# Kernel optimization log

Measured on AMD Instinct MI355X. Metric: run time of the kernel, lower is better.

The kernel has to match this reference:

```python
import jax, jax.numpy as jnp
import numpy as np

SEQ_LEN = 8192
HEAD_DIM = 128


def setup_inputs() -> dict:
    key = jax.random.key(0)
    kq, kk, kv = jax.random.split(key, 3)
    q = jax.random.normal(kq, (SEQ_LEN, HEAD_DIM), dtype=jnp.float32)
    k = jax.random.normal(kk, (SEQ_LEN, HEAD_DIM), dtype=jnp.float32)
    v = jax.random.normal(kv, (SEQ_LEN, HEAD_DIM), dtype=jnp.float32)
    return {"q": q, "k": k, "v": v}


def reference(q, k, v):
    # FlashAttention computes exact softmax attention; the blocked loops with
    # online max/sum rescaling in the source are an exact reformulation of:
    #   O = softmax(Q K^T) V
    # NOTE: the original module applies no 1/sqrt(d) scaling, so neither do we.
    s = jnp.einsum('nd,md->nm', q, k)          # [N, N] scores
    p = jax.nn.softmax(s, axis=-1)             # stable softmax (online in src)
    return jnp.einsum('nm,md->nd', p, v)       # [N, d]
```

## Files before the change

kernel.cpp:

```cpp
#include <hip/hip_runtime.h>

#define N_SEQ 8192
#define HDIM  128

typedef _Float16 half8v  __attribute__((ext_vector_type(8)));
typedef float    floatx16 __attribute__((ext_vector_type(16)));
typedef unsigned int uint32;

__global__ void prep_kv(const float* __restrict__ K, const float* __restrict__ V,
                        _Float16* __restrict__ K16s, _Float16* __restrict__ Vs) {
    __shared__ float Kl[32 * 132];
    __shared__ float Vl[32 * 132];
    const int t  = threadIdx.x;
    const int nt = blockIdx.x;
    const int n0 = nt * 32;
    #pragma unroll
    for (int kk = 0; kk < 4; kk++) {
        int idx = t + 256 * kk;
        int nl = idx >> 5, c4 = idx & 31;
        float4 f = *(((const float4*)(K + (size_t)(n0 + nl) * HDIM)) + c4);
        float* dk = &Kl[nl * 132 + c4 * 4];
        dk[0] = f.x; dk[1] = f.y; dk[2] = f.z; dk[3] = f.w;
        float4 g = *(((const float4*)(V + (size_t)(n0 + nl) * HDIM)) + c4);
        float* dv = &Vl[nl * 132 + c4 * 4];
        dv[0] = g.x; dv[1] = g.y; dv[2] = g.z; dv[3] = g.w;
    }
    __syncthreads();
    #pragma unroll
    for (int rep = 0; rep < 2; rep++) {
        int ch = t + rep * 256;
        int kc = ch >> 6, lane = ch & 63, l31 = lane & 31, q5 = (lane >> 5) & 1;
        half8v h;
        #pragma unroll
        for (int j = 0; j < 8; j++) h[j] = (_Float16)Kl[l31 * 132 + kc * 16 + q5 * 8 + j];
        *(half8v*)(K16s + (((size_t)nt * 8 + kc) * 64 + lane) * 8) = h;
    }
    #pragma unroll
    for (int rep = 0; rep < 2; rep++) {
        int ch = t + rep * 256;
        int dt = ch >> 7, kc2 = (ch >> 6) & 1, lane = ch & 63, l31 = lane & 31, q5 = (lane >> 5) & 1;
        half8v h;
        #pragma unroll
        for (int j = 0; j < 8; j++) h[j] = (_Float16)Vl[(kc2 * 16 + q5 * 8 + j) * 132 + dt * 32 + l31];
        *(half8v*)(Vs + ((((size_t)nt * 4 + dt) * 2 + kc2) * 64 + lane) * 8) = h;
    }
}

static __device__ __forceinline__ void stage_tile(
        const _Float16* __restrict__ K16s, const _Float16* __restrict__ Vs,
        _Float16* lds, size_t nt, int wv, int lane) {
    #pragma unroll
    for (int i = 0; i < 4; i++) {
        const int c = wv * 4 + i;
        const _Float16* base = (c < 8) ? (K16s + (nt * 8 + c) * 512)
                                       : (Vs + (nt * 8 + (size_t)(c - 8)) * 512);
        __builtin_amdgcn_global_load_lds(
            (const __attribute__((address_space(1))) void*)(base + lane * 8),
            (__attribute__((address_space(3))) void*)(lds + c * 512),
            16, 0, 0);
    }
}

static __device__ __forceinline__ void do_pv(const half8v (&vsrc)[8], const uint32 (&hpk)[8],
                                             floatx16 (&oacc)[4], int q5) {
    #pragma unroll
    for (int kc2 = 0; kc2 < 2; kc2++) {
        uint32 pass0 = q5 ? hpk[4 * kc2 + 0] : hpk[4 * kc2 + 2];
        uint32 pass1 = q5 ? hpk[4 * kc2 + 1] : hpk[4 * kc2 + 3];
        uint32 r0 = (uint32)__shfl_xor((int)pass0, 32, 64);
        uint32 r1 = (uint32)__shfl_xor((int)pass1, 32, 64);
        uint32 b0 = q5 ? r0 : hpk[4 * kc2 + 0];
        uint32 b1 = q5 ? r1 : hpk[4 * kc2 + 1];
        uint32 b2 = q5 ? hpk[4 * kc2 + 2] : r0;
        uint32 b3 = q5 ? hpk[4 * kc2 + 3] : r1;
        uint4 bu = make_uint4(b0, b1, b2, b3);
        half8v bfrag = __builtin_bit_cast(half8v, bu);
        #pragma unroll
        for (int dt = 0; dt < 4; dt++)
            oacc[dt] = __builtin_amdgcn_mfma_f32_32x32x16_f16(vsrc[dt * 2 + kc2], bfrag, oacc[dt], 0, 0, 0);
    }
}

template <bool DO_PV>
static __device__ __forceinline__ void pipe_step(
        const half8v (&qf)[8], half8v (&vin)[8], const half8v (&vprev)[8],
        floatx16 (&oacc)[4], uint32 (&hpk)[8],
        float& runm, float& lsum, float& palpha, bool& pflag,
        const _Float16* lds, int lane, int q5) {
    half8v kf[8];
    #pragma unroll
    for (int kc = 0; kc < 8; kc++)
        kf[kc] = *(const half8v*)(lds + kc * 512 + lane * 8);
    #pragma unroll
    for (int j = 0; j < 8; j++)
        vin[j] = *(const half8v*)(lds + (8 + j) * 512 + lane * 8);
    if (pflag) {
        #pragma unroll
        for (int dt = 0; dt < 4; dt++)
            #pragma unroll
            for (int r = 0; r < 16; r++) oacc[dt][r] *= palpha;
        pflag = false;
    }
    if (DO_PV) do_pv(vprev, hpk, oacc, q5);
    floatx16 s0, s1;
    #pragma unroll
    for (int r = 0; r < 16; r++) { s0[r] = 0.0f; s1[r] = 0.0f; }
    #pragma unroll
    for (int kc = 0; kc < 4; kc++)
        s0 = __builtin_amdgcn_mfma_f32_32x32x16_f16(kf[kc], qf[kc], s0, 0, 0, 0);
    #pragma unroll
    for (int kc = 4; kc < 8; kc++)
        s1 = __builtin_amdgcn_mfma_f32_32x32x16_f16(kf[kc], qf[kc], s1, 0, 0, 0);
    float sc[16];
    #pragma unroll
    for (int r = 0; r < 16; r++) sc[r] = s0[r] + s1[r];
    float tm[8];
    #pragma unroll
    for (int r = 0; r < 8; r++) tm[r] = fmaxf(sc[r], sc[r + 8]);
    #pragma unroll
    for (int w = 4; w; w >>= 1)
        #pragma unroll
        for (int r = 0; r < w; r++) tm[r] = fmaxf(tm[r], tm[r + w]);
    float cmax = fmaxf(tm[0], __shfl_xor(tm[0], 32, 64));
    if (__any(cmax > runm + 12.0f)) {
        const float mnew = fmaxf(runm, cmax);
        palpha = __builtin_amdgcn_exp2f(runm - mnew);
        runm = mnew;
        lsum *= palpha;
        pflag = true;
    }
    float p[16];
    #pragma unroll
    for (int r = 0; r < 16; r++) p[r] = __builtin_amdgcn_exp2f(sc[r] - runm);
    float ts[8];
    #pragma unroll
    for (int r = 0; r < 8; r++) ts[r] = p[r] + p[r + 8];
    #pragma unroll
    for (int w = 4; w; w >>= 1)
        #pragma unroll
        for (int r = 0; r < w; r++) ts[r] += ts[r + w];
    lsum += ts[0];
    #pragma unroll
    for (int t2 = 0; t2 < 8; t2++) {
        auto pk = __builtin_amdgcn_cvt_pkrtz(p[2 * t2], p[2 * t2 + 1]);
        hpk[t2] = __builtin_bit_cast(uint32, pk);
    }
}

__launch_bounds__(256, 2)
__global__ void fa_main(const float* __restrict__ Qp, const _Float16* __restrict__ K16s,
                        const _Float16* __restrict__ Vs, float* __restrict__ Opart,
                        float* __restrict__ lpart, float* __restrict__ mpart, int tiles) {
    __shared__ _Float16 ldsbuf[2][8192];
    const int tid  = threadIdx.x;
    const int lane = tid & 63;
    const int wv   = tid >> 6;
    const int l31  = lane & 31;
    const int q5   = lane >> 5;
    const int sp   = blockIdx.x;
    const int m0   = blockIdx.y * 128 + wv * 32;
    const float LOG2E = 1.44269504088896f;

    half8v qf[8];
    {
        const float* qrow = Qp + (size_t)(m0 + l31) * HDIM;
        #pragma unroll
        for (int kc = 0; kc < 8; kc++) {
            const float4 a = *(const float4*)(qrow + kc * 16 + q5 * 8);
            const float4 b = *(const float4*)(qrow + kc * 16 + q5 * 8 + 4);
            half8v h;
            h[0] = (_Float16)(a.x * LOG2E); h[1] = (_Float16)(a.y * LOG2E);
            h[2] = (_Float16)(a.z * LOG2E); h[3] = (_Float16)(a.w * LOG2E);
            h[4] = (_Float16)(b.x * LOG2E); h[5] = (_Float16)(b.y * LOG2E);
            h[6] = (_Float16)(b.z * LOG2E); h[7] = (_Float16)(b.w * LOG2E);
            qf[kc] = h;
        }
    }

    floatx16 oacc[4];
    #pragma unroll
    for (int dt = 0; dt < 4; dt++)
        #pragma unroll
        for (int r = 0; r < 16; r++) oacc[dt][r] = 0.0f;

    float runm = -3.0e38f;
    float lsum = 0.0f;
    float palpha = 0.0f;
    bool  pflag = false;
    uint32 hpk[8];
    half8v va[8], vb[8];

    const size_t nt0 = (size_t)sp * tiles;

    stage_tile(K16s, Vs, ldsbuf[0], nt0, wv, lane);
    __syncthreads();
    stage_tile(K16s, Vs, ldsbuf[1], nt0 + 1, wv, lane);
    pipe_step<false>(qf, va, va, oacc, hpk, runm, lsum, palpha, pflag, ldsbuf[0], lane, q5);
    __syncthreads();
    for (int p = 0; p < (tiles - 2) / 2; p++) {
        stage_tile(K16s, Vs, ldsbuf[0], nt0 + 2 + 2 * p, wv, lane);
        pipe_step<true>(qf, vb, va, oacc, hpk, runm, lsum, palpha, pflag, ldsbuf[1], lane, q5);
        __syncthreads();
        stage_tile(K16s, Vs, ldsbuf[1], nt0 + 3 + 2 * p, wv, lane);
        pipe_step<true>(qf, va, vb, oacc, hpk, runm, lsum, palpha, pflag, ldsbuf[0], lane, q5);
        __syncthreads();
    }
    pipe_step<true>(qf, vb, va, oacc, hpk, runm, lsum, palpha, pflag, ldsbuf[1], lane, q5);
    if (pflag) {
        #pragma unroll
        for (int dt = 0; dt < 4; dt++)
            #pragma unroll
            for (int r = 0; r < 16; r++) oacc[dt][r] *= palpha;
    }
    do_pv(vb, hpk, oacc, q5);

    float ltot = lsum + __shfl_xor(lsum, 32, 64);
    if (lane < 32) {
        __builtin_nontemporal_store(ltot, &lpart[(size_t)sp * N_SEQ + m0 + l31]);
        __builtin_nontemporal_store(runm, &mpart[(size_t)sp * N_SEQ + m0 + l31]);
    }
    #pragma unroll
    for (int dt = 0; dt < 4; dt++)
        #pragma unroll
        for (int r = 0; r < 16; r++) {
            int d = dt * 32 + (r & 3) + 8 * (r >> 2) + 4 * q5;
            __builtin_nontemporal_store(oacc[dt][r],
                &Opart[((size_t)sp * HDIM + d) * N_SEQ + m0 + l31]);
        }
}

__global__ void fa_merge(const float* __restrict__ Opart, const float* __restrict__ lpart,
                         const float* __restrict__ mpart, float* __restrict__ Out, int S) {
    __shared__ float lds[64 * 33];
    const int t  = threadIdx.x;
    const int m0 = blockIdx.x * 64;
    const int i  = t & 63;
    const int g  = t >> 6;
    const int m  = m0 + i;
    const int d0 = blockIdx.y * 32 + g * 8;

    float M = -3.0e38f;
    for (int s = 0; s < S; s++) M = fmaxf(M, mpart[(size_t)s * N_SEQ + m]);
    float L = 0.0f;
    for (int s = 0; s < S; s++)
        L += lpart[(size_t)s * N_SEQ + m] * __builtin_amdgcn_exp2f(mpart[(size_t)s * N_SEQ + m] - M);
    const float inv = 1.0f / L;

    float acc[8];
    #pragma unroll
    for (int dd = 0; dd < 8; dd++) acc[dd] = 0.0f;
    for (int s = 0; s < S; s++) {
        const float ww = __builtin_amdgcn_exp2f(mpart[(size_t)s * N_SEQ + m] - M) * inv;
        #pragma unroll
        for (int dd = 0; dd < 8; dd++)
            acc[dd] += __builtin_nontemporal_load(
                &Opart[((size_t)s * HDIM + d0 + dd) * N_SEQ + m]) * ww;
    }
    #pragma unroll
    for (int dd = 0; dd < 8; dd++) lds[i * 33 + g * 8 + dd] = acc[dd];
    __syncthreads();
    const int mi = t >> 2, c = t & 3;
    float4 v0, v1;
    const float* row = &lds[mi * 33 + c * 8];
    v0.x = row[0]; v0.y = row[1]; v0.z = row[2]; v0.w = row[3];
    v1.x = row[4]; v1.y = row[5]; v1.z = row[6]; v1.w = row[7];
    float* outp = Out + (size_t)(m0 + mi) * HDIM + blockIdx.y * 32 + c * 8;
    *(float4*)(outp)     = v0;
    *(float4*)(outp + 4) = v1;
}

__global__ void fa_naive(const float* __restrict__ Q, const float* __restrict__ K,
                         const float* __restrict__ V, float* __restrict__ O) {
    const int m = blockIdx.x;
    const int t = threadIdx.x;
    __shared__ float qs[HDIM];
    __shared__ float ps[256];
    __shared__ float red[256];
    if (t < HDIM) qs[t] = Q[(size_t)m * HDIM + t] * 1.44269504f;
    __syncthreads();
    float om = -3.0e38f, ls = 0.0f, oa = 0.0f;
    for (int nb = 0; nb < N_SEQ; nb += 256) {
        const float* kr = K + (size_t)(nb + t) * HDIM;
        float s = 0.0f;
        #pragma unroll 8
        for (int d = 0; d < HDIM; d++) s += qs[d] * kr[d];
        red[t] = s; __syncthreads();
        for (int st = 128; st > 0; st >>= 1) { if (t < st) red[t] = fmaxf(red[t], red[t + st]); __syncthreads(); }
        float cm = red[0];
        __syncthreads();
        float mn = fmaxf(om, cm);
        float al = __builtin_amdgcn_exp2f(om - mn);
        om = mn;
        float pp = __builtin_amdgcn_exp2f(s - mn);
        ps[t] = pp; red[t] = pp; __syncthreads();
        for (int st = 128; st > 0; st >>= 1) { if (t < st) red[t] += red[t + st]; __syncthreads(); }
        float csum = red[0];
        ls = ls * al + csum;
        if (t < HDIM) {
            float acc = 0.0f;
            for (int j = 0; j < 256; j++) acc += ps[j] * V[(size_t)(nb + j) * HDIM + t];
            oa = oa * al + acc;
        }
        __syncthreads();
    }
    if (t < HDIM) O[(size_t)m * HDIM + t] = oa / ls;
}

extern "C" void kernel_launch(void* const* d_in, const int* in_sizes, int n_in,
                              void* d_out, int out_size, void* d_ws, size_t ws_size,
                              hipStream_t stream) {
    const float* q = (const float*)d_in[0];
    const float* k = (const float*)d_in[1];
    const float* v = (const float*)d_in[2];
    float* out = (float*)d_out;

    const size_t MB = 1024ull * 1024ull;
    int S = 0;
    for (int s = 8; s >= 1; s >>= 1) {
        size_t need = 4 * MB + (size_t)s * (4 * MB + 64 * 1024);
        if (ws_size >= need) { S = s; break; }
    }
    if (S == 0) {
        fa_naive<<<N_SEQ, 256, 0, stream>>>(q, k, v, out);
        return;
    }
    char* ws = (char*)d_ws;
    _Float16* K16s = (_Float16*)ws;
    _Float16* Vs   = (_Float16*)(ws + 2 * MB);
    float* Opart   = (float*)(ws + 4 * MB);
    float* lpart   = (float*)(ws + 4 * MB + (size_t)S * 4 * MB);
    float* mpart   = lpart + (size_t)S * N_SEQ;

    prep_kv<<<dim3(N_SEQ / 32), dim3(256), 0, stream>>>(k, v, K16s, Vs);
    fa_main<<<dim3(S, N_SEQ / 128), dim3(256), 0, stream>>>(q, K16s, Vs, Opart, lpart, mpart, (N_SEQ / 32) / S);
    fa_merge<<<dim3(N_SEQ / 64, HDIM / 32), dim3(256), 0, stream>>>(Opart, lpart, mpart, out, S);
}
```

Before: 127.7 us.

## Fuse split-KV merge into main kernel via last-block atomic counter

Result: slower. 182.5 us (+42.9%).

```diff
diff --git a/kernel.cpp b/kernel.cpp
--- a/kernel.cpp
+++ b/kernel.cpp
@@ -150,8 +150,10 @@
 __launch_bounds__(256, 2)
 __global__ void fa_main(const float* __restrict__ Qp, const _Float16* __restrict__ K16s,
                         const _Float16* __restrict__ Vs, float* __restrict__ Opart,
-                        float* __restrict__ lpart, float* __restrict__ mpart, int tiles) {
+                        float* __restrict__ lpart, float* __restrict__ mpart,
+                        int* __restrict__ counters, float* __restrict__ Out, int tiles) {
     __shared__ _Float16 ldsbuf[2][8192];
+    __shared__ int is_last_s;
     const int tid  = threadIdx.x;
     const int lane = tid & 63;
     const int wv   = tid >> 6;
@@ -216,57 +218,67 @@
 
     float ltot = lsum + __shfl_xor(lsum, 32, 64);
     if (lane < 32) {
-        __builtin_nontemporal_store(ltot, &lpart[(size_t)sp * N_SEQ + m0 + l31]);
-        __builtin_nontemporal_store(runm, &mpart[(size_t)sp * N_SEQ + m0 + l31]);
+        lpart[(size_t)sp * N_SEQ + m0 + l31] = ltot;
+        mpart[(size_t)sp * N_SEQ + m0 + l31] = runm;
     }
     #pragma unroll
     for (int dt = 0; dt < 4; dt++)
         #pragma unroll
         for (int r = 0; r < 16; r++) {
             int d = dt * 32 + (r & 3) + 8 * (r >> 2) + 4 * q5;
-            __builtin_nontemporal_store(oacc[dt][r],
-                &Opart[((size_t)sp * HDIM + d) * N_SEQ + m0 + l31]);
+            Opart[((size_t)sp * HDIM + d) * N_SEQ + m0 + l31] = oacc[dt][r];
         }
-}
-
-__global__ void fa_merge(const float* __restrict__ Opart, const float* __restrict__ lpart,
-                         const float* __restrict__ mpart, float* __restrict__ Out, int S) {
-    __shared__ float lds[64 * 33];
-    const int t  = threadIdx.x;
-    const int m0 = blockIdx.x * 64;
-    const int i  = t & 63;
-    const int g  = t >> 6;
-    const int m  = m0 + i;
-    const int d0 = blockIdx.y * 32 + g * 8;
-
-    float M = -3.0e38f;
-    for (int s = 0; s < S; s++) M = fmaxf(M, mpart[(size_t)s * N_SEQ + m]);
-    float L = 0.0f;
-    for (int s = 0; s < S; s++)
-        L += lpart[(size_t)s * N_SEQ + m] * __builtin_amdgcn_exp2f(mpart[(size_t)s * N_SEQ + m] - M);
-    const float inv = 1.0f / L;
-
-    float acc[8];
-    #pragma unroll
-    for (int dd = 0; dd < 8; dd++) acc[dd] = 0.0f;
-    for (int s = 0; s < S; s++) {
-        const float ww = __builtin_amdgcn_exp2f(mpart[(size_t)s * N_SEQ + m] - M) * inv;
-        #pragma unroll
-        for (int dd = 0; dd < 8; dd++)
-            acc[dd] += __builtin_nontemporal_load(
-                &Opart[((size_t)s * HDIM + d0 + dd) * N_SEQ + m]) * ww;
-    }
-    #pragma unroll
-    for (int dd = 0; dd < 8; dd++) lds[i * 33 + g * 8 + dd] = acc[dd];
-    __syncthreads();
-    const int mi = t >> 2, c = t & 3;
-    float4 v0, v1;
-    const float* row = &lds[mi * 33 + c * 8];
-    v0.x = row[0]; v0.y = row[1]; v0.z = row[2]; v0.w = row[3];
-    v1.x = row[4]; v1.y = row[5]; v1.z = row[6]; v1.w = row[7];
-    float* outp = Out + (size_t)(m0 + mi) * HDIM + blockIdx.y * 32 + c * 8;
-    *(float4*)(outp)     = v0;
-    *(float4*)(outp + 4) = v1;
+
+    __syncthreads();
+    if (tid == 0) {
+        __threadfence();
+        int old = atomicAdd(&counters[blockIdx.y], 1);
+        is_last_s = (old == (int)gridDim.x - 1);
+    }
+    __syncthreads();
+    if (!is_last_s) return;
+    __threadfence();
+
+    const int S   = gridDim.x;
+    const int ym0 = blockIdx.y * 128;
+    float* ldsf = (float*)ldsbuf;
+    const int i = tid & 63;
+    const int g = tid >> 6;
+    #pragma unroll
+    for (int rh = 0; rh < 2; rh++) {
+        const int m = ym0 + rh * 64 + i;
+        float M = -3.0e38f;
+        for (int s = 0; s < S; s++) M = fmaxf(M, mpart[(size_t)s * N_SEQ + m]);
+        float L = 0.0f;
+        for (int s = 0; s < S; s++)
+            L += lpart[(size_t)s * N_SEQ + m] * __builtin_amdgcn_exp2f(mpart[(size_t)s * N_SEQ + m] - M);
+        const float inv = 1.0f / L;
+        #pragma unroll
+        for (int dg = 0; dg < 4; dg++) {
+            const int d0 = dg * 32 + g * 8;
+            float acc[8];
+            #pragma unroll
+            for (int dd = 0; dd < 8; dd++) acc[dd] = 0.0f;
+            for (int s = 0; s < S; s++) {
+                const float ww = __builtin_amdgcn_exp2f(mpart[(size_t)s * N_SEQ + m] - M) * inv;
+                #pragma unroll
+                for (int dd = 0; dd < 8; dd++)
+                    acc[dd] += Opart[((size_t)s * HDIM + d0 + dd) * N_SEQ + m] * ww;
+            }
+            __syncthreads();
+            #pragma unroll
+            for (int dd = 0; dd < 8; dd++) ldsf[i * 33 + g * 8 + dd] = acc[dd];
+            __syncthreads();
+            const int mi = tid >> 2, c = tid & 3;
+            const float* row = &ldsf[mi * 33 + c * 8];
+            float4 v0, v1;
+            v0.x = row[0]; v0.y = row[1]; v0.z = row[2]; v0.w = row[3];
+            v1.x = row[4]; v1.y = row[5]; v1.z = row[6]; v1.w = row[7];
+            float* outp = Out + (size_t)(ym0 + rh * 64 + mi) * HDIM + dg * 32 + c * 8;
+            *(float4*)(outp)     = v0;
+            *(float4*)(outp + 4) = v1;
+        }
+    }
 }
 
 __global__ void fa_naive(const float* __restrict__ Q, const float* __restrict__ K,
@@ -317,7 +329,7 @@
     const size_t MB = 1024ull * 1024ull;
     int S = 0;
     for (int s = 8; s >= 1; s >>= 1) {
-        size_t need = 4 * MB + (size_t)s * (4 * MB + 64 * 1024);
+        size_t need = 4 * MB + (size_t)s * (4 * MB + 64 * 1024) + 4096;
         if (ws_size >= need) { S = s; break; }
     }
     if (S == 0) {
@@ -330,8 +342,10 @@
     float* Opart   = (float*)(ws + 4 * MB);
     float* lpart   = (float*)(ws + 4 * MB + (size_t)S * 4 * MB);
     float* mpart   = lpart + (size_t)S * N_SEQ;
-
+    int*   counters = (int*)(mpart + (size_t)S * N_SEQ);
+
+    hipMemsetAsync(counters, 0, (N_SEQ / 128) * sizeof(int), stream);
     prep_kv<<<dim3(N_SEQ / 32), dim3(256), 0, stream>>>(k, v, K16s, Vs);
-    fa_main<<<dim3(S, N_SEQ / 128), dim3(256), 0, stream>>>(q, K16s, Vs, Opart, lpart, mpart, (N_SEQ / 32) / S);
-    fa_merge<<<dim3(N_SEQ / 64, HDIM / 32), dim3(256), 0, stream>>>(Opart, lpart, mpart, out, S);
-}
+    fa_main<<<dim3(S, N_SEQ / 128), dim3(256), 0, stream>>>(
+        q, K16s, Vs, Opart, lpart, mpart, counters, out, (N_SEQ / 32) / S);
+}
```
